# Performance work log

Measured on AMD Instinct MI355X. Metric: run time of the kernel, lower is better.

The kernel has to match this reference:

```python
import jax, jax.numpy as jnp
import numpy as np

S, T, B = 32, 48, 1024      # src_len, tgt_len, batch
E, H = 256, 1024            # embedding, hidden
VS, VT = 256, 256           # source/target vocab


def setup_inputs() -> dict:
    key = jax.random.key(0)
    ks = jax.random.split(key, 20)
    s = 0.02
    n = jax.random.normal
    inp = {
        "src": jax.random.randint(ks[0], (S, B), 0, VS),
        "tgt": jax.random.randint(ks[1], (T, B), 0, VT),
        "enc_emb": n(ks[2], (VS, E), jnp.float32) * s,
        "enc_Wih0": n(ks[3], (4 * H, E), jnp.float32) * s,
        "enc_Whh0": n(ks[4], (4 * H, H), jnp.float32) * s,
        "enc_b0": jnp.zeros((4 * H,), jnp.float32),
        "enc_Wih1": n(ks[5], (4 * H, H), jnp.float32) * s,
        "enc_Whh1": n(ks[6], (4 * H, H), jnp.float32) * s,
        "enc_b1": jnp.zeros((4 * H,), jnp.float32),
        "dec_emb": n(ks[7], (VT, E), jnp.float32) * s,
        "dec_Wih0": n(ks[8], (4 * H, E), jnp.float32) * s,
        "dec_Whh0": n(ks[9], (4 * H, H), jnp.float32) * s,
        "dec_b0": jnp.zeros((4 * H,), jnp.float32),
        "dec_Wih1": n(ks[10], (4 * H, H), jnp.float32) * s,
        "dec_Whh1": n(ks[11], (4 * H, H), jnp.float32) * s,
        "dec_b1": jnp.zeros((4 * H,), jnp.float32),
        "fc_W": n(ks[12], (H, VT), jnp.float32) * s,
        "fc_b": jnp.zeros((VT,), jnp.float32),
    }
    return inp


def lstm_step(x, h, c, Wih, Whh, b):
    # PyTorch gate order: i, f, g, o
    z = x @ Wih.T + h @ Whh.T + b
    i, f, g, o = jnp.split(z, 4, axis=-1)
    c = jax.nn.sigmoid(f) * c + jax.nn.sigmoid(i) * jnp.tanh(g)
    h = jax.nn.sigmoid(o) * jnp.tanh(c)
    return h, c


def run_layer(xs, Wih, Whh, b):
    # xs: [S, B, in]; returns all hidden states and final (h, c)
    bsz = xs.shape[1]
    h0 = jnp.zeros((bsz, Whh.shape[1]), xs.dtype)

    def step(carry, x):
        h, c = lstm_step(x, carry[0], carry[1], Wih, Whh, b)
        return (h, c), h

    (h, c), hs = jax.lax.scan(step, (h0, h0), xs)
    return hs, h, c


def reference(src, tgt, enc_emb, enc_Wih0, enc_Whh0, enc_b0, enc_Wih1, enc_Whh1,
              enc_b1, dec_emb, dec_Wih0, dec_Whh0, dec_b0, dec_Wih1, dec_Whh1,
              dec_b1, fc_W, fc_b):
    # ---- Encoder: 2-layer LSTM over source ----
    xe = enc_emb[src]                                   # [S, B, E]
    hs0, h0, c0 = run_layer(xe, enc_Wih0, enc_Whh0, enc_b0)
    _, h1, c1 = run_layer(hs0, enc_Wih1, enc_Whh1, enc_b1)

    # ---- Decoder: per-timestep loop, teacher forcing ratio = 1.0 ----
    def dec_step(carry, tok):
        dh0, dc0, dh1, dc1 = carry
        x = dec_emb[tok]                                # [B, E]
        dh0, dc0 = lstm_step(x, dh0, dc0, dec_Wih0, dec_Whh0, dec_b0)
        dh1, dc1 = lstm_step(dh0, dh1, dc1, dec_Wih1, dec_Whh1, dec_b1)
        logits = dh1 @ fc_W + fc_b                      # [B, VT]
        return (dh0, dc0, dh1, dc1), logits

    _, logits = jax.lax.scan(dec_step, (h0, c0, h1, c1), tgt[:-1])  # [T-1, B, VT]
    # outputs[0] is never written in the original -> stays zeros
    out = jnp.concatenate([jnp.zeros((1,) + logits.shape[1:], logits.dtype), logits], axis=0)
    return out
```

## Files before the change

kernel.cpp:

```cpp
#include <hip/hip_runtime.h>
#include <hip/hip_fp16.h>

typedef __attribute__((ext_vector_type(8))) short short8;
typedef __attribute__((ext_vector_type(4))) float floatx4;

#define DEVFN static __device__ __forceinline__

DEVFN short f2h(float v) { return __half_as_short(__float2half(v)); }

DEVFN void gload16(const void* g, void* l) {
  void* gnc = const_cast<void*>(g);
  __builtin_amdgcn_global_load_lds(
      (__attribute__((address_space(1))) void*)gnc,
      (__attribute__((address_space(3))) void*)l, 16, 0, 0);
}

__global__ __launch_bounds__(256, 2) void pers_kernel(
    short* xe0, short* xe1, short* xd0, short* xd1,
    const short* wc_e0, const short* wc_e1, const short* wc_d0, const short* wc_d1,
    const float* eb0, const float* eb1, const float* db0, const float* db1,
    const short* embe, const short* embd,
    const int* __restrict__ src, const int* __restrict__ tgt,
    short* dh1, unsigned* cells) {
  __shared__ short smem[32768];
  const int tid = threadIdx.x;
  const int lane = tid & 63;
  const int wv = tid >> 6;
  const int wm = wv >> 1;
  const int wu = wv & 1;
  const int l15 = lane & 15;
  const int l4 = lane >> 4;
  const int bx = blockIdx.x;
  const int role1 = bx >> 5;
  const int u0 = (bx & 31) * 32;
  const int gy = blockIdx.y;
  const int m0 = gy * 128;
  const int srow = lane >> 3;
  const int swseg = ((lane & 7) * 16) ^ (srow * 16);
  const long SL0 = 1024l * 1280, SL1 = 1024l * 2048;

  float cst[16];
#pragma unroll
  for (int i = 0; i < 16; ++i) cst[i] = 0.f;

  for (int p = 0; p < 81; ++p) {
    if (p) {
      __syncthreads();
      unsigned* gc = cells + (((long)p * 8 + gy) << 6);
      if (tid == 0)
        __hip_atomic_store(gc + bx, 1u, __ATOMIC_RELEASE, __HIP_MEMORY_SCOPE_AGENT);
      if (tid < 64) {
        while (__hip_atomic_load(gc + tid, __ATOMIC_RELAXED,
                                 __HIP_MEMORY_SCOPE_AGENT) == 0u)
          __builtin_amdgcn_s_sleep(1);
        (void)__hip_atomic_load(gc + tid, __ATOMIC_ACQUIRE, __HIP_MEMORY_SCOPE_AGENT);
      }
      __syncthreads();
    }

    int active, t;
    const int isdec = (p > 32);
    if (!role1) {
      if (!isdec) { active = (p < 32); t = p; }
      else        { active = (p <= 79); t = p - 33; }
    } else {
      if (!isdec) { active = (p >= 1); t = p - 1; }
      else        { active = (p >= 34); t = p - 34; }
    }
    if (!active) continue;

    const int cur = t & 1, nxt = cur ^ 1;
    const short* A; const short* Wt; const float* bs; int ktot;
    short *d1 = nullptr, *d2 = nullptr, *d3 = nullptr, *xq = nullptr;
    int s1 = 0, o1 = 0, xs = 0;
    const short* xe = nullptr; const int* tk = nullptr;
    if (!role1) {
      if (!isdec) {
        A = xe0 + cur * SL0; Wt = wc_e0; bs = eb0; ktot = 1280;
        d2 = xe1 + cur * SL1;
        s1 = 1280; o1 = 256; xs = 1280;
        if (t < 31) { d1 = xe0 + nxt * SL0; xq = d1; xe = embe; tk = src + (t + 1) * 1024; }
        else        { d1 = xd0;             xq = xd0; xe = embd; tk = tgt; }
      } else {
        A = xd0 + cur * SL0; Wt = wc_d0; bs = db0; ktot = 1280;
        d1 = xd0 + nxt * SL0; s1 = 1280; o1 = 256;
        d2 = xd1 + cur * SL1;
        xq = xd0 + nxt * SL0; xs = 1280; xe = embd; tk = tgt + (t + 1) * 1024;
      }
    } else {
      if (!isdec) {
        A = xe1 + cur * SL1; Wt = wc_e1; bs = eb1; ktot = 2048;
        d1 = (t < 31) ? (xe1 + nxt * SL1) : xd1; s1 = 2048; o1 = 1024;
      } else {
        A = xd1 + cur * SL1; Wt = wc_d1; bs = db1; ktot = 2048;
        d1 = xd1 + nxt * SL1; s1 = 2048; o1 = 1024;
        d3 = dh1 + (long)t * 1024 * 1024;
      }
    }

    floatx4 acc[4][4];
#pragma unroll
    for (int g = 0; g < 4; ++g)
#pragma unroll
      for (int mi = 0; mi < 4; ++mi) acc[g][mi] = (floatx4){0.f, 0.f, 0.f, 0.f};

    const char* Ab = (const char*)A;
    const char* Wb = (const char*)Wt;
    const long kbytes = (long)ktot * 2;
    const int nkb = ktot >> 6;

    auto stage = [&](int kb, int bufi) {
      const long kboff = (long)kb * 128;
      short* sb = smem + bufi * 16384;
#pragma unroll
      for (int ci = 0; ci < 8; ++ci) {
        const int c = wv * 8 + ci;
        void* lds = (void*)(sb + c * 512);
        if (c < 16) {
          const int row = c * 8 + srow;
          gload16(Ab + (long)(m0 + row) * kbytes + kboff + swseg, lds);
        } else {
          const int cb = c - 16;
          const int wrow = (cb >> 2) * 1024 + u0 + (cb & 3) * 8 + srow;
          gload16(Wb + (long)wrow * kbytes + kboff + swseg, lds);
        }
      }
    };

    stage(0, 0);
    __syncthreads();
    int buf = 0;
    for (int kb = 0; kb < nkb; ++kb) {
      if (kb + 1 < nkb) stage(kb + 1, buf ^ 1);
      const short* sb = smem + buf * 16384;
#pragma unroll
      for (int k0 = 0; k0 < 64; k0 += 32) {
        short8 fa[4];
        short8 fb[4];
#pragma unroll
        for (int mi = 0; mi < 4; ++mi) {
          const int r = wm * 64 + mi * 16 + l15;
          fa[mi] = *(const short8*)(sb + r * 64 + ((k0 + l4 * 8) ^ ((r & 7) << 3)));
        }
        {
          const int r = wu * 16 + l15;
          const int kk = (k0 + l4 * 8) ^ ((r & 7) << 3);
#pragma unroll
          for (int g = 0; g < 4; ++g)
            fb[g] = *(const short8*)(sb + 8192 + (g * 32 + r) * 64 + kk);
        }
#pragma unroll
        for (int g = 0; g < 4; ++g)
#pragma unroll
          for (int mi = 0; mi < 4; ++mi)
            asm volatile("v_mfma_f32_16x16x32_f16 %0, %1, %2, %0"
                         : "+v"(acc[g][mi])
                         : "v"(fa[mi]), "v"(fb[g]));
      }
      __syncthreads();
      buf ^= 1;
    }
    asm volatile("s_nop 7\ns_nop 7\ns_nop 7");

    const int u = u0 + wu * 16 + l15;
    const float bi = bs[u];
    const float bf_ = bs[1024 + u];
    const float bg = bs[2048 + u];
    const float bo = bs[3072 + u];
    short* ht = smem;
    const int uloc = wu * 16 + l15;
#pragma unroll
    for (int mi = 0; mi < 4; ++mi) {
#pragma unroll
      for (int j = 0; j < 4; ++j) {
        const float zi = acc[0][mi][j] + bi;
        const float zf = acc[1][mi][j] + bf_;
        const float zg = acc[2][mi][j] + bg;
        const float zo = acc[3][mi][j] + bo;
        const float gi = 1.f / (1.f + expf(-zi));
        const float gf = 1.f / (1.f + expf(-zf));
        const float gg = tanhf(zg);
        const float go = 1.f / (1.f + expf(-zo));
        const float cn = gf * cst[mi * 4 + j] + gi * gg;
        cst[mi * 4 + j] = cn;
        const int rl = wm * 64 + mi * 16 + l4 * 4 + j;
        ht[rl * 40 + uloc] = f2h(go * tanhf(cn));
      }
    }
    __syncthreads();

    {
      const int rl = tid >> 1;
      const int seg = (tid & 1) * 16;
      const short8 v0 = *(const short8*)(ht + rl * 40 + seg);
      const short8 v1 = *(const short8*)(ht + rl * 40 + seg + 8);
      const long col = u0 + seg;
      if (d1) {
        short* ptr = d1 + (long)(m0 + rl) * s1 + o1 + col;
        *(short8*)ptr = v0; *(short8*)(ptr + 8) = v1;
      }
      if (d2) {
        short* ptr = d2 + (long)(m0 + rl) * 2048 + col;
        *(short8*)ptr = v0; *(short8*)(ptr + 8) = v1;
      }
      if (d3) {
        short* ptr = d3 + (long)(m0 + rl) * 1024 + col;
        *(short8*)ptr = v0; *(short8*)(ptr + 8) = v1;
      }
    }
    if (xq && bx == 0) {
      for (int i = tid; i < 4096; i += 256) {
        const int row = i >> 5;
        const int e8 = (i & 31) * 8;
        const int b = m0 + row;
        const int tok = tk[b];
        const short8 v = *(const short8*)(xe + (long)tok * 256 + e8);
        *(short8*)(xq + (long)b * xs + e8) = v;
      }
    }
  }
}

__global__ __launch_bounds__(256) void fc_kernel(
    const short* __restrict__ A, const short* __restrict__ W,
    const float* __restrict__ bias, float* __restrict__ outp) {
  __shared__ short smem[32768];
  const int tid = threadIdx.x;
  const int lane = tid & 63;
  const int wv = tid >> 6;
  const int wm = wv >> 1;
  const int wu = wv & 1;
  const int l15 = lane & 15;
  const int l4 = lane >> 4;
  const int u0 = blockIdx.x * 128;
  const int m0 = blockIdx.y * 128;
  const int srow = lane >> 3;
  const int swseg = ((lane & 7) * 16) ^ (srow * 16);

  floatx4 acc[4][4];
#pragma unroll
  for (int g = 0; g < 4; ++g)
#pragma unroll
    for (int mi = 0; mi < 4; ++mi) acc[g][mi] = (floatx4){0.f, 0.f, 0.f, 0.f};

  const char* Ab = (const char*)A;
  const char* Wb = (const char*)W;
  const long kbytes = 2048;
  const int nkb = 16;

  auto stage = [&](int kb, int bufi) {
    const long kboff = (long)kb * 128;
    short* sb = smem + bufi * 16384;
#pragma unroll
    for (int ci = 0; ci < 8; ++ci) {
      const int c = wv * 8 + ci;
      void* lds = (void*)(sb + c * 512);
      if (c < 16) {
        const int row = c * 8 + srow;
        gload16(Ab + (long)(m0 + row) * kbytes + kboff + swseg, lds);
      } else {
        const int cb = c - 16;
        const int wrow = (cb >> 2) * 32 + u0 + (cb & 3) * 8 + srow;
        gload16(Wb + (long)wrow * kbytes + kboff + swseg, lds);
      }
    }
  };

  stage(0, 0);
  __syncthreads();
  int buf = 0;
  for (int kb = 0; kb < nkb; ++kb) {
    if (kb + 1 < nkb) stage(kb + 1, buf ^ 1);
    const short* sb = smem + buf * 16384;
#pragma unroll
    for (int k0 = 0; k0 < 64; k0 += 32) {
      short8 fa[4];
      short8 fb[4];
#pragma unroll
      for (int mi = 0; mi < 4; ++mi) {
        const int r = wm * 64 + mi * 16 + l15;
        fa[mi] = *(const short8*)(sb + r * 64 + ((k0 + l4 * 8) ^ ((r & 7) << 3)));
      }
      {
        const int r = wu * 16 + l15;
        const int kk = (k0 + l4 * 8) ^ ((r & 7) << 3);
#pragma unroll
        for (int g = 0; g < 4; ++g)
          fb[g] = *(const short8*)(sb + 8192 + (g * 32 + r) * 64 + kk);
      }
#pragma unroll
      for (int g = 0; g < 4; ++g)
#pragma unroll
        for (int mi = 0; mi < 4; ++mi)
          asm volatile("v_mfma_f32_16x16x32_f16 %0, %1, %2, %0"
                       : "+v"(acc[g][mi])
                       : "v"(fa[mi]), "v"(fb[g]));
    }
    __syncthreads();
    buf ^= 1;
  }
  asm volatile("s_nop 7\ns_nop 7\ns_nop 7");

#pragma unroll
  for (int g = 0; g < 4; ++g) {
    const int n = u0 + g * 32 + wu * 16 + l15;
    const float bb = bias[n];
#pragma unroll
    for (int mi = 0; mi < 4; ++mi) {
#pragma unroll
      for (int j = 0; j < 4; ++j) {
        const int r = m0 + wm * 64 + mi * 16 + l4 * 4 + j;
        outp[(long)r * 256 + n] = acc[g][mi][j] + bb;
      }
    }
  }
}

__global__ void wprep(const float* __restrict__ A, const float* __restrict__ B,
                      short* __restrict__ dst, int N, int Ka, int Kb) {
  const int ktot = Ka + Kb;
  const int n8 = ktot >> 3;
  const int total = N * n8;
  for (int idx = blockIdx.x * 256 + threadIdx.x; idx < total; idx += gridDim.x * 256) {
    const int n = idx / n8;
    const int k = (idx - n * n8) * 8;
    const float* s = (k < Ka) ? (A + (long)n * Ka + k) : (B + (long)n * Kb + (k - Ka));
    short8 v;
#pragma unroll
    for (int j = 0; j < 8; ++j) v[j] = f2h(s[j]);
    *(short8*)(dst + (long)n * ktot + k) = v;
  }
}

__global__ void embprep(const float* __restrict__ s, short* __restrict__ d, int total8) {
  const int idx = blockIdx.x * 256 + threadIdx.x;
  if (idx >= total8) return;
  short8 v;
#pragma unroll
  for (int j = 0; j < 8; ++j) v[j] = f2h(s[idx * 8 + j]);
  *(short8*)(d + idx * 8) = v;
}

__global__ void fcwprep(const float* __restrict__ fcW, short* __restrict__ dst) {
  const int idx = blockIdx.x * 256 + threadIdx.x;
  const int v = idx & 255;
  const int h = (idx >> 8) * 8;
  short8 o;
#pragma unroll
  for (int j = 0; j < 8; ++j) o[j] = f2h(fcW[(long)(h + j) * 256 + v]);
  *(short8*)(dst + (long)v * 1024 + h) = o;
}

__global__ void initk(const int* __restrict__ src, const float* __restrict__ emb,
                      short* __restrict__ xe0, short* __restrict__ xe1) {
  const int idx = blockIdx.x * 256 + threadIdx.x;
  if (idx < 1024 * 160) {
    const int b = idx / 160;
    const int k = (idx - b * 160) * 8;
    short8 v;
    if (k < 256) {
      const int tok = src[b];
#pragma unroll
      for (int j = 0; j < 8; ++j) v[j] = f2h(emb[(long)tok * 256 + k + j]);
    } else {
#pragma unroll
      for (int j = 0; j < 8; ++j) v[j] = 0;
    }
    *(short8*)(xe0 + (long)b * 1280 + k) = v;
  } else {
    const int i = idx - 1024 * 160;
    if (i < 1024 * 128) {
      const int b = i >> 7;
      const int k = 1024 + (i & 127) * 8;
      short8 v;
#pragma unroll
      for (int j = 0; j < 8; ++j) v[j] = 0;
      *(short8*)(xe1 + (long)b * 2048 + k) = v;
    }
  }
}

extern "C" void kernel_launch(void* const* d_in, const int* in_sizes, int n_in,
                              void* d_out, int out_size, void* d_ws, size_t ws_size,
                              hipStream_t stream) {
  (void)in_sizes; (void)n_in; (void)out_size; (void)ws_size;
  const int* src = (const int*)d_in[0];
  const int* tgt = (const int*)d_in[1];
  const float* enc_emb = (const float*)d_in[2];
  const float* eW0i = (const float*)d_in[3];
  const float* eW0h = (const float*)d_in[4];
  const float* eb0 = (const float*)d_in[5];
  const float* eW1i = (const float*)d_in[6];
  const float* eW1h = (const float*)d_in[7];
  const float* eb1 = (const float*)d_in[8];
  const float* dec_emb = (const float*)d_in[9];
  const float* dW0i = (const float*)d_in[10];
  const float* dW0h = (const float*)d_in[11];
  const float* db0 = (const float*)d_in[12];
  const float* dW1i = (const float*)d_in[13];
  const float* dW1h = (const float*)d_in[14];
  const float* db1 = (const float*)d_in[15];
  const float* fcW = (const float*)d_in[16];
  const float* fcb = (const float*)d_in[17];
  float* out = (float*)d_out;

  char* ws = (char*)d_ws;
  size_t off = 0;
  auto carve = [&](size_t bytes) {
    void* p = ws + off;
    off += (bytes + 255) & ~(size_t)255;
    return p;
  };
  short* wc_e0 = (short*)carve(4096l * 1280 * 2);
  short* wc_e1 = (short*)carve(4096l * 2048 * 2);
  short* wc_d0 = (short*)carve(4096l * 1280 * 2);
  short* wc_d1 = (short*)carve(4096l * 2048 * 2);
  short* fcwt = (short*)carve(256l * 1024 * 2);
  short* embe = (short*)carve(256l * 256 * 2);
  short* embd = (short*)carve(256l * 256 * 2);
  short* xe0 = (short*)carve(2l * 1024 * 1280 * 2);
  short* xe1 = (short*)carve(2l * 1024 * 2048 * 2);
  short* xd0 = (short*)carve(2l * 1024 * 1280 * 2);
  short* xd1 = (short*)carve(2l * 1024 * 2048 * 2);
  short* dh1 = (short*)carve(47l * 1024 * 1024 * 2);
  unsigned* cells = (unsigned*)carve(81l * 8 * 64 * 4);

  hipMemsetAsync(cells, 0, 81l * 8 * 64 * 4, stream);
  hipMemsetAsync(out, 0, 1024l * 256 * 4, stream);

  wprep<<<2560, 256, 0, stream>>>(eW0i, eW0h, wc_e0, 4096, 256, 1024);
  wprep<<<4096, 256, 0, stream>>>(eW1i, eW1h, wc_e1, 4096, 1024, 1024);
  wprep<<<2560, 256, 0, stream>>>(dW0i, dW0h, wc_d0, 4096, 256, 1024);
  wprep<<<4096, 256, 0, stream>>>(dW1i, dW1h, wc_d1, 4096, 1024, 1024);
  embprep<<<32, 256, 0, stream>>>(enc_emb, embe, 8192);
  embprep<<<32, 256, 0, stream>>>(dec_emb, embd, 8192);
  fcwprep<<<128, 256, 0, stream>>>(fcW, fcwt);
  initk<<<1152, 256, 0, stream>>>(src, enc_emb, xe0, xe1);

  pers_kernel<<<dim3(64, 8), 256, 0, stream>>>(
      xe0, xe1, xd0, xd1, wc_e0, wc_e1, wc_d0, wc_d1,
      eb0, eb1, db0, db1, embe, embd, src, tgt, dh1, cells);

  fc_kernel<<<dim3(2, 376), 256, 0, stream>>>(dh1, fcwt, fcb, out + 1024l * 256);
}
```

Before: 4.227 ms.

## Store operands in MFMA fragment-major layout and load directly into registers

```diff
diff --git a/kernel.cpp b/kernel.cpp
--- a/kernel.cpp
+++ b/kernel.cpp
@@ -8,11 +8,8 @@
 
 DEVFN short f2h(float v) { return __half_as_short(__float2half(v)); }
 
-DEVFN void gload16(const void* g, void* l) {
-  void* gnc = const_cast<void*>(g);
-  __builtin_amdgcn_global_load_lds(
-      (__attribute__((address_space(1))) void*)gnc,
-      (__attribute__((address_space(3))) void*)l, 16, 0, 0);
+DEVFN long fmblk(int rblk, int kblk, int nkblk) {
+  return (((long)rblk * nkblk + kblk) << 9);
 }
 
 __global__ __launch_bounds__(256, 2) void pers_kernel(
@@ -22,22 +19,21 @@
     const short* embe, const short* embd,
     const int* __restrict__ src, const int* __restrict__ tgt,
     short* dh1, unsigned* cells) {
-  __shared__ short smem[32768];
+  __shared__ short ht[128 * 40];
   const int tid = threadIdx.x;
   const int lane = tid & 63;
   const int wv = tid >> 6;
   const int wm = wv >> 1;
   const int wu = wv & 1;
   const int l15 = lane & 15;
-  const int l4 = lane >> 4;
+  const int ll4 = lane >> 4;
   const int bx = blockIdx.x;
   const int role1 = bx >> 5;
   const int u0 = (bx & 31) * 32;
   const int gy = blockIdx.y;
   const int m0 = gy * 128;
-  const int srow = lane >> 3;
-  const int swseg = ((lane & 7) * 16) ^ (srow * 16);
   const long SL0 = 1024l * 1280, SL1 = 1024l * 2048;
+  const int lane8 = lane * 8;
 
   float cst[16];
 #pragma unroll
@@ -104,62 +100,47 @@
 #pragma unroll
       for (int mi = 0; mi < 4; ++mi) acc[g][mi] = (floatx4){0.f, 0.f, 0.f, 0.f};
 
-    const char* Ab = (const char*)A;
-    const char* Wb = (const char*)Wt;
-    const long kbytes = (long)ktot * 2;
+    const int nkblk = ktot >> 5;
     const int nkb = ktot >> 6;
-
-    auto stage = [&](int kb, int bufi) {
-      const long kboff = (long)kb * 128;
-      short* sb = smem + bufi * 16384;
-#pragma unroll
-      for (int ci = 0; ci < 8; ++ci) {
-        const int c = wv * 8 + ci;
-        void* lds = (void*)(sb + c * 512);
-        if (c < 16) {
-          const int row = c * 8 + srow;
-          gload16(Ab + (long)(m0 + row) * kbytes + kboff + swseg, lds);
-        } else {
-          const int cb = c - 16;
-          const int wrow = (cb >> 2) * 1024 + u0 + (cb & 3) * 8 + srow;
-          gload16(Wb + (long)wrow * kbytes + kboff + swseg, lds);
-        }
-      }
-    };
-
-    stage(0, 0);
-    __syncthreads();
-    int buf = 0;
-    for (int kb = 0; kb < nkb; ++kb) {
-      if (kb + 1 < nkb) stage(kb + 1, buf ^ 1);
-      const short* sb = smem + buf * 16384;
-#pragma unroll
-      for (int k0 = 0; k0 < 64; k0 += 32) {
-        short8 fa[4];
-        short8 fb[4];
-#pragma unroll
-        for (int mi = 0; mi < 4; ++mi) {
-          const int r = wm * 64 + mi * 16 + l15;
-          fa[mi] = *(const short8*)(sb + r * 64 + ((k0 + l4 * 8) ^ ((r & 7) << 3)));
-        }
-        {
-          const int r = wu * 16 + l15;
-          const int kk = (k0 + l4 * 8) ^ ((r & 7) << 3);
-#pragma unroll
-          for (int g = 0; g < 4; ++g)
-            fb[g] = *(const short8*)(sb + 8192 + (g * 32 + r) * 64 + kk);
-        }
-#pragma unroll
-        for (int g = 0; g < 4; ++g)
-#pragma unroll
-          for (int mi = 0; mi < 4; ++mi)
-            asm volatile("v_mfma_f32_16x16x32_f16 %0, %1, %2, %0"
-                         : "+v"(acc[g][mi])
-                         : "v"(fa[mi]), "v"(fb[g]));
-      }
-      __syncthreads();
-      buf ^= 1;
-    }
+    const int arblk = (m0 >> 4) + wm * 4;
+    const int wrblk = (u0 >> 4) + wu;
+
+    short8 a0[8], w0[8], a1[8], w1[8];
+
+#define LOADT(AB, WB, kb)                                                      \
+  do {                                                                         \
+    _Pragma("unroll") for (int mi = 0; mi < 4; ++mi)                           \
+      _Pragma("unroll") for (int h = 0; h < 2; ++h)                            \
+        AB[mi * 2 + h] =                                                       \
+            *(const short8*)(A + fmblk(arblk + mi, (kb) * 2 + h, nkblk) + lane8); \
+    _Pragma("unroll") for (int g = 0; g < 4; ++g)                              \
+      _Pragma("unroll") for (int h = 0; h < 2; ++h)                            \
+        WB[g * 2 + h] =                                                        \
+            *(const short8*)(Wt + fmblk(wrblk + g * 64, (kb) * 2 + h, nkblk) + lane8); \
+  } while (0)
+
+#define MFMAT(AB, WB)                                                          \
+  do {                                                                         \
+    _Pragma("unroll") for (int h = 0; h < 2; ++h)                              \
+      _Pragma("unroll") for (int g = 0; g < 4; ++g)                            \
+        _Pragma("unroll") for (int mi = 0; mi < 4; ++mi)                       \
+          asm volatile("v_mfma_f32_16x16x32_f16 %0, %1, %2, %0"                \
+                       : "+v"(acc[g][mi])                                      \
+                       : "v"(AB[mi * 2 + h]), "v"(WB[g * 2 + h]));             \
+  } while (0)
+
+    LOADT(a0, w0, 0);
+    int kb = 0;
+    while (true) {
+      if (kb + 1 < nkb) LOADT(a1, w1, kb + 1);
+      MFMAT(a0, w0);
+      ++kb; if (kb >= nkb) break;
+      if (kb + 1 < nkb) LOADT(a0, w0, kb + 1);
+      MFMAT(a1, w1);
+      ++kb; if (kb >= nkb) break;
+    }
+#undef LOADT
+#undef MFMAT
     asm volatile("s_nop 7\ns_nop 7\ns_nop 7");
 
     const int u = u0 + wu * 16 + l15;
@@ -167,7 +148,6 @@
     const float bf_ = bs[1024 + u];
     const float bg = bs[2048 + u];
     const float bo = bs[3072 + u];
-    short* ht = smem;
     const int uloc = wu * 16 + l15;
 #pragma unroll
     for (int mi = 0; mi < 4; ++mi) {
@@ -183,39 +163,44 @@
         const float go = 1.f / (1.f + expf(-zo));
         const float cn = gf * cst[mi * 4 + j] + gi * gg;
         cst[mi * 4 + j] = cn;
-        const int rl = wm * 64 + mi * 16 + l4 * 4 + j;
+        const int rl = wm * 64 + mi * 16 + ll4 * 4 + j;
         ht[rl * 40 + uloc] = f2h(go * tanhf(cn));
       }
     }
     __syncthreads();
 
     {
-      const int rl = tid >> 1;
-      const int seg = (tid & 1) * 16;
-      const short8 v0 = *(const short8*)(ht + rl * 40 + seg);
-      const short8 v1 = *(const short8*)(ht + rl * 40 + seg + 8);
-      const long col = u0 + seg;
+      const int rb = tid >> 5;
+      const int c = tid & 31;
+      const int l4w = c >> 3;
+      const int pr = c & 7;
+      const int r0 = rb * 16 + pr * 2;
+      const short8 v0 = *(const short8*)(ht + r0 * 40 + l4w * 8);
+      const short8 v1 = *(const short8*)(ht + (r0 + 1) * 40 + l4w * 8);
+      const int rgb = (m0 >> 4) + rb;
+      const int inner = l4w * 128 + pr * 16;
       if (d1) {
-        short* ptr = d1 + (long)(m0 + rl) * s1 + o1 + col;
-        *(short8*)ptr = v0; *(short8*)(ptr + 8) = v1;
+        long ix = fmblk(rgb, (o1 + u0) >> 5, s1 >> 5) + inner;
+        *(short8*)(d1 + ix) = v0; *(short8*)(d1 + ix + 8) = v1;
       }
       if (d2) {
-        short* ptr = d2 + (long)(m0 + rl) * 2048 + col;
-        *(short8*)ptr = v0; *(short8*)(ptr + 8) = v1;
+        long ix = fmblk(rgb, u0 >> 5, 64) + inner;
+        *(short8*)(d2 + ix) = v0; *(short8*)(d2 + ix + 8) = v1;
       }
       if (d3) {
-        short* ptr = d3 + (long)(m0 + rl) * 1024 + col;
-        *(short8*)ptr = v0; *(short8*)(ptr + 8) = v1;
+        long ix = fmblk(rgb, u0 >> 5, 32) + inner;
+        *(short8*)(d3 + ix) = v0; *(short8*)(d3 + ix + 8) = v1;
       }
     }
     if (xq && bx == 0) {
+      const int xnk = xs >> 5;
       for (int i = tid; i < 4096; i += 256) {
-        const int row = i >> 5;
-        const int e8 = (i & 31) * 8;
-        const int b = m0 + row;
-        const int tok = tk[b];
-        const short8 v = *(const short8*)(xe + (long)tok * 256 + e8);
-        *(short8*)(xq + (long)b * xs + e8) = v;
+        const int bl = i >> 5;
+        const int c = i & 31;
+        const int tok = tk[m0 + bl];
+        const short8 v = *(const short8*)(xe + (long)tok * 256 + c * 8);
+        long ix = fmblk((m0 + bl) >> 4, c >> 2, xnk) + (c & 3) * 128 + (bl & 15) * 8;
+        *(short8*)(xq + ix) = v;
       }
     }
   }
@@ -224,18 +209,16 @@
 __global__ __launch_bounds__(256) void fc_kernel(
     const short* __restrict__ A, const short* __restrict__ W,
     const float* __restrict__ bias, float* __restrict__ outp) {
-  __shared__ short smem[32768];
   const int tid = threadIdx.x;
   const int lane = tid & 63;
   const int wv = tid >> 6;
   const int wm = wv >> 1;
   const int wu = wv & 1;
   const int l15 = lane & 15;
-  const int l4 = lane >> 4;
+  const int ll4 = lane >> 4;
   const int u0 = blockIdx.x * 128;
   const int m0 = blockIdx.y * 128;
-  const int srow = lane >> 3;
-  const int swseg = ((lane & 7) * 16) ^ (srow * 16);
+  const int lane8 = lane * 8;
 
   floatx4 acc[4][4];
 #pragma unroll
@@ -243,62 +226,43 @@
 #pragma unroll
     for (int mi = 0; mi < 4; ++mi) acc[g][mi] = (floatx4){0.f, 0.f, 0.f, 0.f};
 
-  const char* Ab = (const char*)A;
-  const char* Wb = (const char*)W;
-  const long kbytes = 2048;
-  const int nkb = 16;
-
-  auto stage = [&](int kb, int bufi) {
-    const long kboff = (long)kb * 128;
-    short* sb = smem + bufi * 16384;
-#pragma unroll
-    for (int ci = 0; ci < 8; ++ci) {
-      const int c = wv * 8 + ci;
-      void* lds = (void*)(sb + c * 512);
-      if (c < 16) {
-        const int row = c * 8 + srow;
-        gload16(Ab + (long)(m0 + row) * kbytes + kboff + swseg, lds);
-      } else {
-        const int cb = c - 16;
-        const int wrow = (cb >> 2) * 32 + u0 + (cb & 3) * 8 + srow;
-        gload16(Wb + (long)wrow * kbytes + kboff + swseg, lds);
-      }
-    }
-  };
-
-  stage(0, 0);
-  __syncthreads();
-  int buf = 0;
-  for (int kb = 0; kb < nkb; ++kb) {
-    if (kb + 1 < nkb) stage(kb + 1, buf ^ 1);
-    const short* sb = smem + buf * 16384;
-#pragma unroll
-    for (int k0 = 0; k0 < 64; k0 += 32) {
-      short8 fa[4];
-      short8 fb[4];
-#pragma unroll
-      for (int mi = 0; mi < 4; ++mi) {
-        const int r = wm * 64 + mi * 16 + l15;
-        fa[mi] = *(const short8*)(sb + r * 64 + ((k0 + l4 * 8) ^ ((r & 7) << 3)));
-      }
-      {
-        const int r = wu * 16 + l15;
-        const int kk = (k0 + l4 * 8) ^ ((r & 7) << 3);
-#pragma unroll
-        for (int g = 0; g < 4; ++g)
-          fb[g] = *(const short8*)(sb + 8192 + (g * 32 + r) * 64 + kk);
-      }
-#pragma unroll
-      for (int g = 0; g < 4; ++g)
-#pragma unroll
-        for (int mi = 0; mi < 4; ++mi)
-          asm volatile("v_mfma_f32_16x16x32_f16 %0, %1, %2, %0"
-                       : "+v"(acc[g][mi])
-                       : "v"(fa[mi]), "v"(fb[g]));
-    }
-    __syncthreads();
-    buf ^= 1;
+  const int nkblk = 32, nkb = 16;
+  const int arblk = (m0 >> 4) + wm * 4;
+  const int wrblk = (u0 >> 4) + wu;
+
+  short8 a0[8], w0[8], a1[8], w1[8];
+#define LOADT(AB, WB, kb)                                                      \
+  do {                                                                         \
+    _Pragma("unroll") for (int mi = 0; mi < 4; ++mi)                           \
+      _Pragma("unroll") for (int h = 0; h < 2; ++h)                            \
+        AB[mi * 2 + h] =                                                       \
+            *(const short8*)(A + fmblk(arblk + mi, (kb) * 2 + h, nkblk) + lane8); \
+    _Pragma("unroll") for (int g = 0; g < 4; ++g)                              \
+      _Pragma("unroll") for (int h = 0; h < 2; ++h)                            \
+        WB[g * 2 + h] =                                                        \
+            *(const short8*)(W + fmblk(wrblk + g * 2, (kb) * 2 + h, nkblk) + lane8); \
+  } while (0)
+#define MFMAT(AB, WB)                                                          \
+  do {                                                                         \
+    _Pragma("unroll") for (int h = 0; h < 2; ++h)                              \
+      _Pragma("unroll") for (int g = 0; g < 4; ++g)                            \
+        _Pragma("unroll") for (int mi = 0; mi < 4; ++mi)                       \
+          asm volatile("v_mfma_f32_16x16x32_f16 %0, %1, %2, %0"                \
+                       : "+v"(acc[g][mi])                                      \
+                       : "v"(AB[mi * 2 + h]), "v"(WB[g * 2 + h]));             \
+  } while (0)
+  LOADT(a0, w0, 0);
+  int kb = 0;
+  while (true) {
+    if (kb + 1 < nkb) LOADT(a1, w1, kb + 1);
+    MFMAT(a0, w0);
+    ++kb; if (kb >= nkb) break;
+    if (kb + 1 < nkb) LOADT(a0, w0, kb + 1);
+    MFMAT(a1, w1);
+    ++kb; if (kb >= nkb) break;
   }
+#undef LOADT
+#undef MFMAT
   asm volatile("s_nop 7\ns_nop 7\ns_nop 7");
 
 #pragma unroll
@@ -309,7 +273,7 @@
     for (int mi = 0; mi < 4; ++mi) {
 #pragma unroll
       for (int j = 0; j < 4; ++j) {
-        const int r = m0 + wm * 64 + mi * 16 + l4 * 4 + j;
+        const int r = m0 + wm * 64 + mi * 16 + ll4 * 4 + j;
         outp[(long)r * 256 + n] = acc[g][mi][j] + bb;
       }
     }
@@ -321,6 +285,7 @@
   const int ktot = Ka + Kb;
   const int n8 = ktot >> 3;
   const int total = N * n8;
+  const int nkblk = ktot >> 5;
   for (int idx = blockIdx.x * 256 + threadIdx.x; idx < total; idx += gridDim.x * 256) {
     const int n = idx / n8;
     const int k = (idx - n * n8) * 8;
@@ -328,7 +293,8 @@
     short8 v;
 #pragma unroll
     for (int j = 0; j < 8; ++j) v[j] = f2h(s[j]);
-    *(short8*)(dst + (long)n * ktot + k) = v;
+    long ix = fmblk(n >> 4, k >> 5, nkblk) + ((k >> 3) & 3) * 128 + (n & 15) * 8;
+    *(short8*)(dst + ix) = v;
   }
 }
 
@@ -348,7 +314,8 @@
   short8 o;
 #pragma unroll
   for (int j = 0; j < 8; ++j) o[j] = f2h(fcW[(long)(h + j) * 256 + v]);
-  *(short8*)(dst + (long)v * 1024 + h) = o;
+  long ix = fmblk(v >> 4, h >> 5, 32) + ((h >> 3) & 3) * 128 + (v & 15) * 8;
+  *(short8*)(dst + ix) = o;
 }
 
 __global__ void initk(const int* __restrict__ src, const float* __restrict__ emb,
@@ -366,7 +333,8 @@
 #pragma unroll
       for (int j = 0; j < 8; ++j) v[j] = 0;
     }
-    *(short8*)(xe0 + (long)b * 1280 + k) = v;
+    long ix = fmblk(b >> 4, k >> 5, 40) + ((k >> 3) & 3) * 128 + (b & 15) * 8;
+    *(short8*)(xe0 + ix) = v;
   } else {
     const int i = idx - 1024 * 160;
     if (i < 1024 * 128) {
@@ -375,7 +343,8 @@
       short8 v;
 #pragma unroll
       for (int j = 0; j < 8; ++j) v[j] = 0;
-      *(short8*)(xe1 + (long)b * 2048 + k) = v;
+      long ix = fmblk(b >> 4, k >> 5, 64) + ((k >> 3) & 3) * 128 + (b & 15) * 8;
+      *(short8*)(xe1 + ix) = v;
     }
   }
 }
```

Measured after the change: 10.68 ms. +152.6%, slower.

## Replace global per-phase barrier with per-role dependency flags in persistent LSTM kernel

Applied to the files above, without the earlier changes.

```diff
diff --git a/kernel.cpp b/kernel.cpp
--- a/kernel.cpp
+++ b/kernel.cpp
@@ -13,6 +13,10 @@
   __builtin_amdgcn_global_load_lds(
       (__attribute__((address_space(1))) void*)gnc,
       (__attribute__((address_space(3))) void*)l, 16, 0, 0);
+}
+
+DEVFN unsigned* fset(unsigned* f, int role, int s, int gy) {
+  return f + ((((role * 79) + s) * 8 + gy) << 5);
 }
 
 __global__ __launch_bounds__(256, 2) void pers_kernel(
@@ -21,7 +25,7 @@
     const float* eb0, const float* eb1, const float* db0, const float* db1,
     const short* embe, const short* embd,
     const int* __restrict__ src, const int* __restrict__ tgt,
-    short* dh1, unsigned* cells) {
+    short* dh1, unsigned* flags) {
   __shared__ short smem[32768];
   const int tid = threadIdx.x;
   const int lane = tid & 63;
@@ -32,7 +36,8 @@
   const int l4 = lane >> 4;
   const int bx = blockIdx.x;
   const int role1 = bx >> 5;
-  const int u0 = (bx & 31) * 32;
+  const int ut = bx & 31;
+  const int u0 = ut * 32;
   const int gy = blockIdx.y;
   const int m0 = gy * 128;
   const int srow = lane >> 3;
@@ -43,39 +48,39 @@
 #pragma unroll
   for (int i = 0; i < 16; ++i) cst[i] = 0.f;
 
-  for (int p = 0; p < 81; ++p) {
-    if (p) {
+  for (int s = 0; s < 79; ++s) {
+    unsigned* WA = nullptr;
+    unsigned* WB = nullptr;
+    if (!role1) {
+      if (s >= 1) WA = fset(flags, 0, s - 1, gy);
+      if (s >= 2) WB = fset(flags, 1, s - 2, gy);
+    } else {
+      WA = fset(flags, 0, s, gy);
+      if (s >= 1) WB = fset(flags, 1, s - 1, gy);
+    }
+    if (WA || WB) {
+      if (tid < 64) {
+        unsigned* p = (tid < 32) ? (WA ? WA + tid : nullptr)
+                                 : (WB ? WB + (tid - 32) : nullptr);
+        if (p) {
+          while (__hip_atomic_load(p, __ATOMIC_RELAXED,
+                                   __HIP_MEMORY_SCOPE_AGENT) == 0u)
+            __builtin_amdgcn_s_sleep(1);
+          (void)__hip_atomic_load(p, __ATOMIC_ACQUIRE, __HIP_MEMORY_SCOPE_AGENT);
+        }
+      }
       __syncthreads();
-      unsigned* gc = cells + (((long)p * 8 + gy) << 6);
-      if (tid == 0)
-        __hip_atomic_store(gc + bx, 1u, __ATOMIC_RELEASE, __HIP_MEMORY_SCOPE_AGENT);
-      if (tid < 64) {
-        while (__hip_atomic_load(gc + tid, __ATOMIC_RELAXED,
-                                 __HIP_MEMORY_SCOPE_AGENT) == 0u)
-          __builtin_amdgcn_s_sleep(1);
-        (void)__hip_atomic_load(gc + tid, __ATOMIC_ACQUIRE, __HIP_MEMORY_SCOPE_AGENT);
-      }
-      __syncthreads();
-    }
-
-    int active, t;
-    const int isdec = (p > 32);
-    if (!role1) {
-      if (!isdec) { active = (p < 32); t = p; }
-      else        { active = (p <= 79); t = p - 33; }
-    } else {
-      if (!isdec) { active = (p >= 1); t = p - 1; }
-      else        { active = (p >= 34); t = p - 34; }
-    }
-    if (!active) continue;
-
+    }
+
+    const int enc = (s < 32) ? 1 : 0;
+    const int t = enc ? s : s - 32;
     const int cur = t & 1, nxt = cur ^ 1;
     const short* A; const short* Wt; const float* bs; int ktot;
     short *d1 = nullptr, *d2 = nullptr, *d3 = nullptr, *xq = nullptr;
     int s1 = 0, o1 = 0, xs = 0;
     const short* xe = nullptr; const int* tk = nullptr;
     if (!role1) {
-      if (!isdec) {
+      if (enc) {
         A = xe0 + cur * SL0; Wt = wc_e0; bs = eb0; ktot = 1280;
         d2 = xe1 + cur * SL1;
         s1 = 1280; o1 = 256; xs = 1280;
@@ -85,10 +90,10 @@
         A = xd0 + cur * SL0; Wt = wc_d0; bs = db0; ktot = 1280;
         d1 = xd0 + nxt * SL0; s1 = 1280; o1 = 256;
         d2 = xd1 + cur * SL1;
-        xq = xd0 + nxt * SL0; xs = 1280; xe = embd; tk = tgt + (t + 1) * 1024;
+        if (t < 46) { xq = xd0 + nxt * SL0; xs = 1280; xe = embd; tk = tgt + (t + 1) * 1024; }
       }
     } else {
-      if (!isdec) {
+      if (enc) {
         A = xe1 + cur * SL1; Wt = wc_e1; bs = eb1; ktot = 2048;
         d1 = (t < 31) ? (xe1 + nxt * SL1) : xd1; s1 = 2048; o1 = 1024;
       } else {
@@ -196,28 +201,32 @@
       const short8 v1 = *(const short8*)(ht + rl * 40 + seg + 8);
       const long col = u0 + seg;
       if (d1) {
-        short* ptr = d1 + (long)(m0 + rl) * s1 + o1 + col;
-        *(short8*)ptr = v0; *(short8*)(ptr + 8) = v1;
+        short* p = d1 + (long)(m0 + rl) * s1 + o1 + col;
+        *(short8*)p = v0; *(short8*)(p + 8) = v1;
       }
       if (d2) {
-        short* ptr = d2 + (long)(m0 + rl) * 2048 + col;
-        *(short8*)ptr = v0; *(short8*)(ptr + 8) = v1;
+        short* p = d2 + (long)(m0 + rl) * 2048 + col;
+        *(short8*)p = v0; *(short8*)(p + 8) = v1;
       }
       if (d3) {
-        short* ptr = d3 + (long)(m0 + rl) * 1024 + col;
-        *(short8*)ptr = v0; *(short8*)(ptr + 8) = v1;
-      }
-    }
-    if (xq && bx == 0) {
-      for (int i = tid; i < 4096; i += 256) {
-        const int row = i >> 5;
-        const int e8 = (i & 31) * 8;
-        const int b = m0 + row;
-        const int tok = tk[b];
-        const short8 v = *(const short8*)(xe + (long)tok * 256 + e8);
-        *(short8*)(xq + (long)b * xs + e8) = v;
-      }
-    }
+        short* p = d3 + (long)(m0 + rl) * 1024 + col;
+        *(short8*)p = v0; *(short8*)(p + 8) = v1;
+      }
+    }
+    if (xq && tid < 128) {
+      const int i = ut * 128 + tid;
+      const int row = i >> 5;
+      const int e8 = (i & 31) * 8;
+      const int b = m0 + row;
+      const int tok = tk[b];
+      const short8 v = *(const short8*)(xe + (long)tok * 256 + e8);
+      *(short8*)(xq + (long)b * xs + e8) = v;
+    }
+
+    __syncthreads();
+    if (tid == 0)
+      __hip_atomic_store(fset(flags, role1, s, gy) + ut, 1u,
+                         __ATOMIC_RELEASE, __HIP_MEMORY_SCOPE_AGENT);
   }
 }
 
@@ -423,9 +432,10 @@
   short* xd0 = (short*)carve(2l * 1024 * 1280 * 2);
   short* xd1 = (short*)carve(2l * 1024 * 2048 * 2);
   short* dh1 = (short*)carve(47l * 1024 * 1024 * 2);
-  unsigned* cells = (unsigned*)carve(81l * 8 * 64 * 4);
-
-  hipMemsetAsync(cells, 0, 81l * 8 * 64 * 4, stream);
+  const size_t flagbytes = 2l * 79 * 8 * 32 * 4;
+  unsigned* flags = (unsigned*)carve(flagbytes);
+
+  hipMemsetAsync(flags, 0, flagbytes, stream);
   hipMemsetAsync(out, 0, 1024l * 256 * 4, stream);
 
   wprep<<<2560, 256, 0, stream>>>(eW0i, eW0h, wc_e0, 4096, 256, 1024);
@@ -439,7 +449,7 @@
 
   pers_kernel<<<dim3(64, 8), 256, 0, stream>>>(
       xe0, xe1, xd0, xd1, wc_e0, wc_e1, wc_d0, wc_d1,
-      eb0, eb1, db0, db1, embe, embd, src, tgt, dh1, cells);
+      eb0, eb1, db0, db1, embe, embd, src, tgt, dh1, flags);
 
   fc_kernel<<<dim3(2, 376), 256, 0, stream>>>(dh1, fcwt, fcb, out + 1024l * 256);
 }
```

New measurement: 4.210 ms. Within noise of the previous version (-0.4%).
